# Kernel optimization log

Measured on AMD Instinct MI355X. Metric: run time of the kernel, lower is better.

Reference implementation:

```python
import jax, jax.numpy as jnp
import numpy as np
from jax import lax

DIM = 192
HEADS = 8
B, H, W = 2, 256, 256
EPS = 1e-12  # F.normalize default eps


def conv1x1(x, w):
    # x: [b, ci, h, w], w: [co, ci]
    return jnp.einsum('oi,bihw->bohw', w, x)


def dwconv3x3(x, w):
    # depthwise 3x3, SAME padding; w: [c, 1, 3, 3]
    c = x.shape[1]
    return lax.conv_general_dilated(
        x, w, window_strides=(1, 1), padding='SAME',
        dimension_numbers=('NCHW', 'OIHW', 'NCHW'),
        feature_group_count=c)


def l2norm(x):
    # F.normalize over last axis
    n = jnp.sqrt(jnp.sum(x * x, axis=-1, keepdims=True))
    return x / jnp.maximum(n, EPS)


def setup_inputs() -> dict:
    key = jax.random.key(0)
    ks = jax.random.split(key, 8)
    s = 0.02
    return {
        'x': jax.random.normal(ks[0], (B, DIM, H, W), jnp.float32),
        'x_ref': jax.random.normal(ks[1], (B, DIM, H, W), jnp.float32),
        'wq': jax.random.normal(ks[2], (DIM, DIM), jnp.float32) * s,
        'wq_dw': jax.random.normal(ks[3], (DIM, 1, 3, 3), jnp.float32) * s,
        'wkv': jax.random.normal(ks[4], (2 * DIM, DIM), jnp.float32) * s,
        'wkv_dw': jax.random.normal(ks[5], (2 * DIM, 1, 3, 3), jnp.float32) * s,
        'wproj': jax.random.normal(ks[6], (DIM, DIM), jnp.float32) * s,
        'temperature': jnp.ones((HEADS, 1, 1), jnp.float32),
    }


def reference(x, x_ref, wq, wq_dw, wkv, wkv_dw, wproj, temperature):
    b, c, h, w = x.shape
    ch = c // HEADS  # channels per head
    hw = h * w

    q = dwconv3x3(conv1x1(x, wq), wq_dw)            # [b, c, h, w]
    kv = dwconv3x3(conv1x1(x_ref, wkv), wkv_dw)      # [b, 2c, h, w]
    k, v = jnp.split(kv, 2, axis=1)

    q = q.reshape(b, HEADS, ch, hw)
    k = k.reshape(b, HEADS, ch, hw)
    v = v.reshape(b, HEADS, ch, hw)

    q = l2norm(q)
    k = l2norm(k)

    # channel-wise attention: [b, head, ch, ch]
    attn = jnp.einsum('bhcn,bhdn->bhcd', q, k) * temperature
    attn = jax.nn.softmax(attn, axis=-1)
    out = jnp.einsum('bhcd,bhdn->bhcn', attn, v)     # [b, head, ch, hw]

    out = out.reshape(b, c, h, w)
    out = conv1x1(out, wproj)
    return out
```

## Files before the change

### kernel.cpp

```cpp
#include <hip/hip_runtime.h>
#include <hip/hip_bf16.h>

#define B_ 2
#define C_ 192
#define HEADS_ 8
#define CH_ 24
#define H_ 256
#define W_ 256
#define HW_ 65536


using bf16x8 = __attribute__((ext_vector_type(8))) __bf16;
using f32x4  = __attribute__((ext_vector_type(4))) float;

__device__ __forceinline__ float b2f_us(unsigned short u) {
    return __uint_as_float(((unsigned)u) << 16);
}
__device__ __forceinline__ unsigned short f2bf(float f) {
    union { __hip_bfloat16 b; unsigned short u; } cv;
    cv.b = __float2bfloat16(f);
    return cv.u;
}

__global__ __launch_bounds__(256) void convert_w(
    const float* __restrict__ wq, const float* __restrict__ wkv,
    unsigned short* __restrict__ wqbf, unsigned short* __restrict__ wkvbf)
{
    int i = blockIdx.x * 256 + threadIdx.x;
    const float* src; unsigned short* dst; int qd;
    if (i < 9216) { src = wq;  dst = wqbf;  qd = i; }
    else          { src = wkv; dst = wkvbf; qd = i - 9216; }
    float4 v = *(const float4*)(src + (size_t)qd * 4);
    ushort4 u;
    u.x = f2bf(v.x); u.y = f2bf(v.y); u.z = f2bf(v.z); u.w = f2bf(v.w);
    *(ushort4*)(dst + (size_t)qd * 4) = u;
}

template<bool B_F32, bool OUT_F32>
__global__ __launch_bounds__(256) void gemm_mfma(
    const unsigned short* __restrict__ A, long a_bstride,
    const void* __restrict__ Bv, void* __restrict__ Outv, int outC)
{
    const int nb = blockIdx.x * 64;
    const int mt = blockIdx.y;
    const int b  = blockIdx.z;
    const int t  = threadIdx.x;

    __shared__ unsigned short Bl[2][64 * 40];

    const unsigned short* Ab = A + (size_t)b * a_bstride + (size_t)mt * 192 * 192;
    const int w = t >> 6, l = t & 63, li = l & 15, q = l >> 4;
    const int p0 = (t & 15) * 4;
    const int kp = t >> 4;

    const float* Bf = (const float*)Bv + (size_t)b * 192 * HW_;
    const unsigned short* Bh = (const unsigned short*)Bv + (size_t)b * 192 * HW_;

    float4  rf[2][2];
    ushort4 rh[2][2];
    bf16x8  af[2][3];

    auto LOADB = [&](int kc) {
        const int set = kc & 1;
        const size_t off = (size_t)(kc * 32 + kp * 2) * HW_ + nb + p0;
        if constexpr (B_F32) {
            rf[set][0] = *(const float4*)(Bf + off);
            rf[set][1] = *(const float4*)(Bf + off + HW_);
        } else {
            rh[set][0] = *(const ushort4*)(Bh + off);
            rh[set][1] = *(const ushort4*)(Bh + off + HW_);
        }
    };
    auto CVTW = [&](int kc) {
        const int set = kc & 1;
        unsigned pk2[4];
        if constexpr (B_F32) {
            pk2[0] = (unsigned)f2bf(rf[set][0].x) | ((unsigned)f2bf(rf[set][1].x) << 16);
            pk2[1] = (unsigned)f2bf(rf[set][0].y) | ((unsigned)f2bf(rf[set][1].y) << 16);
            pk2[2] = (unsigned)f2bf(rf[set][0].z) | ((unsigned)f2bf(rf[set][1].z) << 16);
            pk2[3] = (unsigned)f2bf(rf[set][0].w) | ((unsigned)f2bf(rf[set][1].w) << 16);
        } else {
            pk2[0] = (unsigned)rh[set][0].x | ((unsigned)rh[set][1].x << 16);
            pk2[1] = (unsigned)rh[set][0].y | ((unsigned)rh[set][1].y << 16);
            pk2[2] = (unsigned)rh[set][0].z | ((unsigned)rh[set][1].z << 16);
            pk2[3] = (unsigned)rh[set][0].w | ((unsigned)rh[set][1].w << 16);
        }
        unsigned short* dst = &Bl[set][kp * 2];
#pragma unroll
        for (int c4 = 0; c4 < 4; c4++) {
            int p = p0 + c4;
            int rB = ((p & 3) << 4) | (p >> 2);
            *(unsigned int*)&dst[rB * 40] = pk2[c4];
        }
    };
    auto AFLOAD = [&](int kc) {
#pragma unroll
        for (int mi = 0; mi < 3; mi++)
            af[kc & 1][mi] = *(const bf16x8*)(Ab + (size_t)(w * 48 + mi * 16 + li) * 192
                                                 + kc * 32 + q * 8);
    };

    f32x4 acc[3][4];
#pragma unroll
    for (int mi = 0; mi < 3; mi++)
#pragma unroll
        for (int ni = 0; ni < 4; ni++)
            acc[mi][ni] = (f32x4){0.f, 0.f, 0.f, 0.f};

    LOADB(0);
    LOADB(1);
    AFLOAD(0);
    CVTW(0);
    asm volatile("s_waitcnt lgkmcnt(0)" ::: "memory");
    __builtin_amdgcn_s_barrier();

#pragma unroll
    for (int c = 0; c < 6; c++) {
        if (c + 1 < 6) AFLOAD(c + 1);
        if (c + 2 < 6) LOADB(c + 2);

        bf16x8 bfr[4];
#pragma unroll
        for (int ni = 0; ni < 4; ni++)
            bfr[ni] = *(const bf16x8*)&Bl[c & 1][(ni * 16 + li) * 40 + q * 8];
#pragma unroll
        for (int mi = 0; mi < 3; mi++)
#pragma unroll
            for (int ni = 0; ni < 4; ni++)
                acc[mi][ni] = __builtin_amdgcn_mfma_f32_16x16x32_bf16(
                    af[c & 1][mi], bfr[ni], acc[mi][ni], 0, 0, 0);

        if (c + 1 < 6) {
            CVTW(c + 1);
            asm volatile("s_waitcnt lgkmcnt(0)" ::: "memory");
            __builtin_amdgcn_s_barrier();
        }
    }

    if (OUT_F32) {
        float* Ob = (float*)Outv + ((size_t)b * outC + (size_t)mt * 192) * HW_;
#pragma unroll
        for (int mi = 0; mi < 3; mi++)
#pragma unroll
            for (int r = 0; r < 4; r++) {
                int o = w * 48 + mi * 16 + q * 4 + r;
                float4 vv;
                vv.x = acc[mi][0][r]; vv.y = acc[mi][1][r];
                vv.z = acc[mi][2][r]; vv.w = acc[mi][3][r];
                *(float4*)(Ob + (size_t)o * HW_ + nb + 4 * li) = vv;
            }
    } else {
        unsigned short* Ob = (unsigned short*)Outv + ((size_t)b * outC + (size_t)mt * 192) * HW_;
#pragma unroll
        for (int mi = 0; mi < 3; mi++)
#pragma unroll
            for (int r = 0; r < 4; r++) {
                int o = w * 48 + mi * 16 + q * 4 + r;
                ushort4 u;
                u.x = f2bf(acc[mi][0][r]); u.y = f2bf(acc[mi][1][r]);
                u.z = f2bf(acc[mi][2][r]); u.w = f2bf(acc[mi][3][r]);
                *(ushort4*)(Ob + (size_t)o * HW_ + nb + 4 * li) = u;
            }
    }
}

#define VYG 4
__global__ __launch_bounds__(256) void dwconv_v(
    const __hip_bfloat16* __restrict__ tmpKV, const float* __restrict__ wkv_dw,
    __hip_bfloat16* __restrict__ V)
{
    const int y0 = blockIdx.x * VYG, cg = blockIdx.y, b = blockIdx.z;
    const int t = threadIdx.x;
    const int c = cg * 32 + (t >> 3);
    const int x0 = (t & 7) * 32;
    const unsigned short* base =
        (const unsigned short*)(tmpKV + ((size_t)b * 2 * C_ + C_ + c) * HW_);
    const float* wp = wkv_dw + (size_t)(C_ + c) * 9;
    float wgt[9];
#pragma unroll
    for (int i = 0; i < 9; i++) wgt[i] = wp[i];

    for (int yi = 0; yi < VYG; yi++) {
        const int y = y0 + yi;
        float o[32];
#pragma unroll
        for (int i = 0; i < 32; i++) o[i] = 0.f;

#pragma unroll
        for (int dy = -1; dy <= 1; dy++) {
            int yy = y + dy;
            if ((unsigned)yy >= 256u) continue;
            const unsigned short* r = base + yy * W_;
            float v[34];
            v[0]  = (x0 > 0) ? b2f_us(r[x0 - 1]) : 0.f;
            v[33] = (x0 + 32 < 256) ? b2f_us(r[x0 + 32]) : 0.f;
            const uint4* r4 = (const uint4*)(r + x0);
#pragma unroll
            for (int m = 0; m < 4; m++) {
                uint4 raw = r4[m];
                unsigned u;
                u = raw.x; v[1 + 8*m + 0] = __uint_as_float(u << 16); v[1 + 8*m + 1] = __uint_as_float(u & 0xffff0000u);
                u = raw.y; v[1 + 8*m + 2] = __uint_as_float(u << 16); v[1 + 8*m + 3] = __uint_as_float(u & 0xffff0000u);
                u = raw.z; v[1 + 8*m + 4] = __uint_as_float(u << 16); v[1 + 8*m + 5] = __uint_as_float(u & 0xffff0000u);
                u = raw.w; v[1 + 8*m + 6] = __uint_as_float(u << 16); v[1 + 8*m + 7] = __uint_as_float(u & 0xffff0000u);
            }
            float w0 = wgt[3 * (dy + 1) + 0];
            float w1 = wgt[3 * (dy + 1) + 1];
            float w2 = wgt[3 * (dy + 1) + 2];
#pragma unroll
            for (int i = 0; i < 32; i++)
                o[i] += v[i] * w0 + v[i + 1] * w1 + v[i + 2] * w2;
        }
        unsigned short* dst = (unsigned short*)V + ((size_t)b * C_ + c) * HW_ + y * W_ + x0;
#pragma unroll
        for (int m = 0; m < 4; m++) {
            uint4 pk;
            pk.x = (unsigned)f2bf(o[8*m + 0]) | ((unsigned)f2bf(o[8*m + 1]) << 16);
            pk.y = (unsigned)f2bf(o[8*m + 2]) | ((unsigned)f2bf(o[8*m + 3]) << 16);
            pk.z = (unsigned)f2bf(o[8*m + 4]) | ((unsigned)f2bf(o[8*m + 5]) << 16);
            pk.w = (unsigned)f2bf(o[8*m + 6]) | ((unsigned)f2bf(o[8*m + 7]) << 16);
            *(uint4*)(dst + 8 * m) = pk;
        }
    }
}

#define PADB 264
#define YG 4
__global__ __launch_bounds__(256) void dw_qk_gram(
    const __hip_bfloat16* __restrict__ tmpQ,
    const __hip_bfloat16* __restrict__ tmpKV,
    const float* __restrict__ wq_dw, const float* __restrict__ wkv_dw,
    float* __restrict__ G, float* __restrict__ sq, float* __restrict__ sk)
{
    const int y0 = blockIdx.x * YG, h = blockIdx.y, b = blockIdx.z;
    const int t = threadIdx.x;

    __shared__ unsigned short Qs[CH_ * PADB];
    __shared__ unsigned short Ks[CH_ * PADB];
    __shared__ float sqs[CH_], sks[CH_];

    if (t < CH_) { sqs[t] = 0.f; sks[t] = 0.f; }

    const int w = t >> 6, l = t & 63, li = l & 15, q = l >> 4;
    const int tr = w >> 1, tc = w & 1;
    int ar = tr * 16 + li; if (ar > 23) ar = 23;
    int br = tc * 16 + li; if (br > 23) br = 23;
    const unsigned short* arow = &Qs[ar * PADB];
    const unsigned short* brow = &Ks[br * PADB];
    f32x4 acc = (f32x4){0.f, 0.f, 0.f, 0.f};

    __syncthreads();

    for (int yi = 0; yi < YG; yi++) {
        const int y = y0 + yi;

        for (int u = t; u < 384; u += 256) {
            const int tens = (u >= 192);
            const int rem = u - tens * 192;
            const int c = rem >> 3;
            const int x0 = (rem & 7) * 32;
            const unsigned short* base = tens
                ? (const unsigned short*)(tmpKV + ((size_t)b * 2 * C_ + h * CH_ + c) * HW_)
                : (const unsigned short*)(tmpQ  + ((size_t)b * C_     + h * CH_ + c) * HW_);
            const float* wp = (tens ? wkv_dw : wq_dw) + (size_t)(h * CH_ + c) * 9;

            float o[32];
#pragma unroll
            for (int i = 0; i < 32; i++) o[i] = 0.f;

#pragma unroll
            for (int dy = -1; dy <= 1; dy++) {
                int yy = y + dy;
                if ((unsigned)yy >= 256u) continue;
                const unsigned short* r = base + yy * W_;
                float v[34];
                v[0]  = (x0 > 0) ? b2f_us(r[x0 - 1]) : 0.f;
                v[33] = (x0 + 32 < 256) ? b2f_us(r[x0 + 32]) : 0.f;
                const uint4* r4 = (const uint4*)(r + x0);
#pragma unroll
                for (int m = 0; m < 4; m++) {
                    uint4 raw = r4[m];
                    unsigned uu;
                    uu = raw.x; v[1 + 8*m + 0] = __uint_as_float(uu << 16); v[1 + 8*m + 1] = __uint_as_float(uu & 0xffff0000u);
                    uu = raw.y; v[1 + 8*m + 2] = __uint_as_float(uu << 16); v[1 + 8*m + 3] = __uint_as_float(uu & 0xffff0000u);
                    uu = raw.z; v[1 + 8*m + 4] = __uint_as_float(uu << 16); v[1 + 8*m + 5] = __uint_as_float(uu & 0xffff0000u);
                    uu = raw.w; v[1 + 8*m + 6] = __uint_as_float(uu << 16); v[1 + 8*m + 7] = __uint_as_float(uu & 0xffff0000u);
                }
                float w0 = wp[3 * (dy + 1) + 0];
                float w1 = wp[3 * (dy + 1) + 1];
                float w2 = wp[3 * (dy + 1) + 2];
#pragma unroll
                for (int i = 0; i < 32; i++)
                    o[i] += v[i] * w0 + v[i + 1] * w1 + v[i + 2] * w2;
            }

            float s = 0.f;
#pragma unroll
            for (int i = 0; i < 32; i++) s += o[i] * o[i];
            atomicAdd(tens ? &sks[c] : &sqs[c], s);

            unsigned short* dst = (tens ? Ks : Qs) + c * PADB + x0;
#pragma unroll
            for (int m = 0; m < 4; m++) {
                uint4 pk;
                pk.x = (unsigned)f2bf(o[8*m + 0]) | ((unsigned)f2bf(o[8*m + 1]) << 16);
                pk.y = (unsigned)f2bf(o[8*m + 2]) | ((unsigned)f2bf(o[8*m + 3]) << 16);
                pk.z = (unsigned)f2bf(o[8*m + 4]) | ((unsigned)f2bf(o[8*m + 5]) << 16);
                pk.w = (unsigned)f2bf(o[8*m + 6]) | ((unsigned)f2bf(o[8*m + 7]) << 16);
                *(uint4*)(dst + 8 * m) = pk;
            }
        }
        __syncthreads();

#pragma unroll
        for (int ks = 0; ks < 8; ks++) {
            bf16x8 af = *(const bf16x8*)&arow[ks * 32 + q * 8];
            bf16x8 bf = *(const bf16x8*)&brow[ks * 32 + q * 8];
            acc = __builtin_amdgcn_mfma_f32_16x16x32_bf16(af, bf, acc, 0, 0, 0);
        }
        __syncthreads();
    }

    if (t < CH_) {
        atomicAdd(&sq[b * C_ + h * CH_ + t], sqs[t]);
        atomicAdd(&sk[b * C_ + h * CH_ + t], sks[t]);
    }

    float* Gb = G + (size_t)(b * HEADS_ + h) * CH_ * CH_;
    const int col = tc * 16 + li;
    if (col < CH_) {
#pragma unroll
        for (int r = 0; r < 4; r++) {
            int row = tr * 16 + q * 4 + r;
            if (row < CH_)
                atomicAdd(&Gb[row * CH_ + col], acc[r]);
        }
    }
}

__global__ __launch_bounds__(192) void softmax_proj(
    const float* __restrict__ G, const float* __restrict__ sq,
    const float* __restrict__ sk, const float* __restrict__ temperature,
    const float* __restrict__ wproj, unsigned short* __restrict__ Mbf)
{
    const int h = blockIdx.x, b = blockIdx.y, t = threadIdx.x;
    __shared__ float attn[CH_][CH_];
    __shared__ float rk[CH_];
    const float* Gb = G + (size_t)(b * HEADS_ + h) * CH_ * CH_;
    if (t < CH_)
        rk[t] = 1.f / fmaxf(sqrtf(sk[b * C_ + h * CH_ + t]), 1e-12f);
    __syncthreads();
    if (t < CH_) {
        float rq = 1.f / fmaxf(sqrtf(sq[b * C_ + h * CH_ + t]), 1e-12f);
        float tempv = temperature[h];
        float row[CH_];
        float mx = -1e30f;
        for (int d = 0; d < CH_; d++) {
            row[d] = Gb[t * CH_ + d] * rq * rk[d] * tempv;
            mx = fmaxf(mx, row[d]);
        }
        float s = 0.f;
        for (int d = 0; d < CH_; d++) { row[d] = __expf(row[d] - mx); s += row[d]; }
        float inv = 1.f / s;
        for (int d = 0; d < CH_; d++) attn[t][d] = row[d] * inv;
    }
    __syncthreads();
    const int o = t;
    float wrow[CH_];
    for (int c = 0; c < CH_; c++) wrow[c] = wproj[o * C_ + h * CH_ + c];
    for (int d = 0; d < CH_; d++) {
        float s = 0.f;
        for (int c = 0; c < CH_; c++) s += wrow[c] * attn[c][d];
        Mbf[((size_t)b * C_ + o) * C_ + h * CH_ + d] = f2bf(s);
    }
}

extern "C" void kernel_launch(void* const* d_in, const int* in_sizes, int n_in,
                              void* d_out, int out_size, void* d_ws, size_t ws_size,
                              hipStream_t stream)
{
    const float* x           = (const float*)d_in[0];
    const float* x_ref       = (const float*)d_in[1];
    const float* wq          = (const float*)d_in[2];
    const float* wq_dw       = (const float*)d_in[3];
    const float* wkv         = (const float*)d_in[4];
    const float* wkv_dw      = (const float*)d_in[5];
    const float* wproj       = (const float*)d_in[6];
    const float* temperature = (const float*)d_in[7];
    float* out = (float*)d_out;

    char* ws = (char*)d_ws;
    __hip_bfloat16* tmpQ  = (__hip_bfloat16*)(ws);
    __hip_bfloat16* tmpKV = (__hip_bfloat16*)(ws + 50331648);
    __hip_bfloat16* tmpV  = (__hip_bfloat16*)(ws);
    float* G  = (float*)(ws + 150994944);
    float* sq = (float*)(ws + 151031808);
    float* sk = (float*)(ws + 151033344);
    unsigned short* wqbf  = (unsigned short*)(ws + 151034880);
    unsigned short* wkvbf = (unsigned short*)(ws + 151108608);
    unsigned short* Mbf   = (unsigned short*)(ws + 151034880);

    hipMemsetAsync(G, 0, 36864 + 1536 + 1536, stream);

    convert_w<<<dim3(108), 256, 0, stream>>>(wq, wkv, wqbf, wkvbf);
    gemm_mfma<true, false><<<dim3(HW_ / 64, 1, B_), 256, 0, stream>>>(
        wqbf, 0, x, tmpQ, 192);
    gemm_mfma<true, false><<<dim3(HW_ / 64, 2, B_), 256, 0, stream>>>(
        wkvbf, 0, x_ref, tmpKV, 384);
    dw_qk_gram<<<dim3(H_ / YG, HEADS_, B_), 256, 0, stream>>>(
        tmpQ, tmpKV, wq_dw, wkv_dw, G, sq, sk);
    softmax_proj<<<dim3(HEADS_, B_), 192, 0, stream>>>(
        G, sq, sk, temperature, wproj, Mbf);
    dwconv_v<<<dim3(H_ / VYG, 6, B_), 256, 0, stream>>>(tmpKV, wkv_dw, tmpV);
    gemm_mfma<false, true><<<dim3(HW_ / 64, 1, B_), 256, 0, stream>>>(
        Mbf, 192 * 192, tmpV, out, 192);
}
```

Measured before the change: 444.3 us.

## Retile 1x1-conv GEMM to 96 output channels by 256 pixels per block

Measured after the change: 443.4 us. No clear change (-0.2%).

```diff
diff --git a/kernel.cpp b/kernel.cpp
--- a/kernel.cpp
+++ b/kernel.cpp
@@ -41,94 +41,101 @@
     const unsigned short* __restrict__ A, long a_bstride,
     const void* __restrict__ Bv, void* __restrict__ Outv, int outC)
 {
-    const int nb = blockIdx.x * 64;
+    const int nb0 = blockIdx.x * 256;
     const int mt = blockIdx.y;
     const int b  = blockIdx.z;
     const int t  = threadIdx.x;
 
-    __shared__ unsigned short Bl[2][64 * 40];
-
-    const unsigned short* Ab = A + (size_t)b * a_bstride + (size_t)mt * 192 * 192;
+    __shared__ unsigned short Bl[2][4][64 * 40];
+
+    const unsigned short* Ab = A + (size_t)b * a_bstride + (size_t)mt * 96 * 192;
     const int w = t >> 6, l = t & 63, li = l & 15, q = l >> 4;
-    const int p0 = (t & 15) * 4;
-    const int kp = t >> 4;
+
+    const int ps  = (t & 63) * 4;
+    const int sub = ps >> 6;
+    const int pin = ps & 63;
+    const int kw  = (t >> 6) * 2;
 
     const float* Bf = (const float*)Bv + (size_t)b * 192 * HW_;
     const unsigned short* Bh = (const unsigned short*)Bv + (size_t)b * 192 * HW_;
 
-    float4  rf[2][2];
-    ushort4 rh[2][2];
-    bf16x8  af[2][3];
+    float4  rf[2][8];
+    ushort4 rh[2][8];
+    bf16x8  af[6];
 
     auto LOADB = [&](int kc) {
         const int set = kc & 1;
-        const size_t off = (size_t)(kc * 32 + kp * 2) * HW_ + nb + p0;
-        if constexpr (B_F32) {
-            rf[set][0] = *(const float4*)(Bf + off);
-            rf[set][1] = *(const float4*)(Bf + off + HW_);
-        } else {
-            rh[set][0] = *(const ushort4*)(Bh + off);
-            rh[set][1] = *(const ushort4*)(Bh + off + HW_);
+#pragma unroll
+        for (int j = 0; j < 4; j++) {
+            const int k = kc * 32 + kw + j * 8;
+            const size_t off = (size_t)k * HW_ + nb0 + ps;
+            if constexpr (B_F32) {
+                rf[set][2*j]   = *(const float4*)(Bf + off);
+                rf[set][2*j+1] = *(const float4*)(Bf + off + HW_);
+            } else {
+                rh[set][2*j]   = *(const ushort4*)(Bh + off);
+                rh[set][2*j+1] = *(const ushort4*)(Bh + off + HW_);
+            }
         }
     };
     auto CVTW = [&](int kc) {
         const int set = kc & 1;
-        unsigned pk2[4];
-        if constexpr (B_F32) {
-            pk2[0] = (unsigned)f2bf(rf[set][0].x) | ((unsigned)f2bf(rf[set][1].x) << 16);
-            pk2[1] = (unsigned)f2bf(rf[set][0].y) | ((unsigned)f2bf(rf[set][1].y) << 16);
-            pk2[2] = (unsigned)f2bf(rf[set][0].z) | ((unsigned)f2bf(rf[set][1].z) << 16);
-            pk2[3] = (unsigned)f2bf(rf[set][0].w) | ((unsigned)f2bf(rf[set][1].w) << 16);
-        } else {
-            pk2[0] = (unsigned)rh[set][0].x | ((unsigned)rh[set][1].x << 16);
-            pk2[1] = (unsigned)rh[set][0].y | ((unsigned)rh[set][1].y << 16);
-            pk2[2] = (unsigned)rh[set][0].z | ((unsigned)rh[set][1].z << 16);
-            pk2[3] = (unsigned)rh[set][0].w | ((unsigned)rh[set][1].w << 16);
-        }
-        unsigned short* dst = &Bl[set][kp * 2];
-#pragma unroll
-        for (int c4 = 0; c4 < 4; c4++) {
-            int p = p0 + c4;
-            int rB = ((p & 3) << 4) | (p >> 2);
-            *(unsigned int*)&dst[rB * 40] = pk2[c4];
+#pragma unroll
+        for (int j = 0; j < 4; j++) {
+            const int kk = kw + j * 8;
+            unsigned pk2[4];
+            if constexpr (B_F32) {
+                pk2[0] = (unsigned)f2bf(rf[set][2*j].x) | ((unsigned)f2bf(rf[set][2*j+1].x) << 16);
+                pk2[1] = (unsigned)f2bf(rf[set][2*j].y) | ((unsigned)f2bf(rf[set][2*j+1].y) << 16);
+                pk2[2] = (unsigned)f2bf(rf[set][2*j].z) | ((unsigned)f2bf(rf[set][2*j+1].z) << 16);
+                pk2[3] = (unsigned)f2bf(rf[set][2*j].w) | ((unsigned)f2bf(rf[set][2*j+1].w) << 16);
+            } else {
+                pk2[0] = (unsigned)rh[set][2*j].x | ((unsigned)rh[set][2*j+1].x << 16);
+                pk2[1] = (unsigned)rh[set][2*j].y | ((unsigned)rh[set][2*j+1].y << 16);
+                pk2[2] = (unsigned)rh[set][2*j].z | ((unsigned)rh[set][2*j+1].z << 16);
+                pk2[3] = (unsigned)rh[set][2*j].w | ((unsigned)rh[set][2*j+1].w << 16);
+            }
+#pragma unroll
+            for (int c4 = 0; c4 < 4; c4++) {
+                int rB = (c4 << 4) | (pin >> 2);
+                *(unsigned int*)&Bl[set][sub][rB * 40 + kk] = pk2[c4];
+            }
         }
     };
     auto AFLOAD = [&](int kc) {
 #pragma unroll
-        for (int mi = 0; mi < 3; mi++)
-            af[kc & 1][mi] = *(const bf16x8*)(Ab + (size_t)(w * 48 + mi * 16 + li) * 192
-                                                 + kc * 32 + q * 8);
+        for (int mi = 0; mi < 6; mi++)
+            af[mi] = *(const bf16x8*)(Ab + (size_t)(mi * 16 + li) * 192 + kc * 32 + q * 8);
     };
 
-    f32x4 acc[3][4];
-#pragma unroll
-    for (int mi = 0; mi < 3; mi++)
+    f32x4 acc[6][4];
+#pragma unroll
+    for (int mi = 0; mi < 6; mi++)
 #pragma unroll
         for (int ni = 0; ni < 4; ni++)
             acc[mi][ni] = (f32x4){0.f, 0.f, 0.f, 0.f};
 
     LOADB(0);
     LOADB(1);
-    AFLOAD(0);
     CVTW(0);
     asm volatile("s_waitcnt lgkmcnt(0)" ::: "memory");
     __builtin_amdgcn_s_barrier();
 
 #pragma unroll
     for (int c = 0; c < 6; c++) {
-        if (c + 1 < 6) AFLOAD(c + 1);
+        AFLOAD(c);
         if (c + 2 < 6) LOADB(c + 2);
 
         bf16x8 bfr[4];
 #pragma unroll
         for (int ni = 0; ni < 4; ni++)
-            bfr[ni] = *(const bf16x8*)&Bl[c & 1][(ni * 16 + li) * 40 + q * 8];
-#pragma unroll
-        for (int mi = 0; mi < 3; mi++)
+            bfr[ni] = *(const bf16x8*)&Bl[c & 1][w][(ni * 16 + li) * 40 + q * 8];
+#pragma unroll
+        for (int mi = 0; mi < 6; mi++)
 #pragma unroll
             for (int ni = 0; ni < 4; ni++)
                 acc[mi][ni] = __builtin_amdgcn_mfma_f32_16x16x32_bf16(
-                    af[c & 1][mi], bfr[ni], acc[mi][ni], 0, 0, 0);
+                    af[mi], bfr[ni], acc[mi][ni], 0, 0, 0);
 
         if (c + 1 < 6) {
             CVTW(c + 1);
@@ -138,28 +145,28 @@
     }
 
     if (OUT_F32) {
-        float* Ob = (float*)Outv + ((size_t)b * outC + (size_t)mt * 192) * HW_;
-#pragma unroll
-        for (int mi = 0; mi < 3; mi++)
+        float* Ob = (float*)Outv + ((size_t)b * outC + (size_t)mt * 96) * HW_;
+#pragma unroll
+        for (int mi = 0; mi < 6; mi++)
 #pragma unroll
             for (int r = 0; r < 4; r++) {
-                int o = w * 48 + mi * 16 + q * 4 + r;
+                int o = mi * 16 + q * 4 + r;
                 float4 vv;
                 vv.x = acc[mi][0][r]; vv.y = acc[mi][1][r];
                 vv.z = acc[mi][2][r]; vv.w = acc[mi][3][r];
-                *(float4*)(Ob + (size_t)o * HW_ + nb + 4 * li) = vv;
+                *(float4*)(Ob + (size_t)o * HW_ + nb0 + w * 64 + 4 * li) = vv;
             }
     } else {
-        unsigned short* Ob = (unsigned short*)Outv + ((size_t)b * outC + (size_t)mt * 192) * HW_;
-#pragma unroll
-        for (int mi = 0; mi < 3; mi++)
+        unsigned short* Ob = (unsigned short*)Outv + ((size_t)b * outC + (size_t)mt * 96) * HW_;
+#pragma unroll
+        for (int mi = 0; mi < 6; mi++)
 #pragma unroll
             for (int r = 0; r < 4; r++) {
-                int o = w * 48 + mi * 16 + q * 4 + r;
+                int o = mi * 16 + q * 4 + r;
                 ushort4 u;
                 u.x = f2bf(acc[mi][0][r]); u.y = f2bf(acc[mi][1][r]);
                 u.z = f2bf(acc[mi][2][r]); u.w = f2bf(acc[mi][3][r]);
-                *(ushort4*)(Ob + (size_t)o * HW_ + nb + 4 * li) = u;
+                *(ushort4*)(Ob + (size_t)o * HW_ + nb0 + w * 64 + 4 * li) = u;
             }
     }
 }
@@ -403,15 +410,15 @@
     hipMemsetAsync(G, 0, 36864 + 1536 + 1536, stream);
 
     convert_w<<<dim3(108), 256, 0, stream>>>(wq, wkv, wqbf, wkvbf);
-    gemm_mfma<true, false><<<dim3(HW_ / 64, 1, B_), 256, 0, stream>>>(
+    gemm_mfma<true, false><<<dim3(HW_ / 256, 2, B_), 256, 0, stream>>>(
         wqbf, 0, x, tmpQ, 192);
-    gemm_mfma<true, false><<<dim3(HW_ / 64, 2, B_), 256, 0, stream>>>(
+    gemm_mfma<true, false><<<dim3(HW_ / 256, 4, B_), 256, 0, stream>>>(
         wkvbf, 0, x_ref, tmpKV, 384);
     dw_qk_gram<<<dim3(H_ / YG, HEADS_, B_), 256, 0, stream>>>(
         tmpQ, tmpKV, wq_dw, wkv_dw, G, sq, sk);
     softmax_proj<<<dim3(HEADS_, B_), 192, 0, stream>>>(
         G, sq, sk, temperature, wproj, Mbf);
     dwconv_v<<<dim3(H_ / VYG, 6, B_), 256, 0, stream>>>(tmpKV, wkv_dw, tmpV);
-    gemm_mfma<false, true><<<dim3(HW_ / 64, 1, B_), 256, 0, stream>>>(
+    gemm_mfma<false, true><<<dim3(HW_ / 256, 2, B_), 256, 0, stream>>>(
         Mbf, 192 * 192, tmpV, out, 192);
 }
```
